# Performance work log

Hardware: AMD Instinct MI355X
Metric: run time of the kernel (lower is better)

Reference implementation:

```python
import jax, jax.numpy as jnp
import numpy as np

ALPHA = 0.1  # leakyRNN default alpha


def setup_inputs() -> dict:
    key = jax.random.key(0)
    k1, k2, k3, k4 = jax.random.split(key, 4)
    B, T, N_in, n, N = 256, 2048, 3, 2, 128
    u = jax.random.normal(k1, (B, T, N_in), dtype=jnp.float32)
    matB = jax.random.uniform(k2, (N, N), dtype=jnp.float32)
    # scaled for recurrence stability over T=2048 steps (spectral radius of 0.9*I + 0.1*W < 1)
    wIn = jax.random.normal(k3, (n, N_in), dtype=jnp.float32) * 0.5
    wRec = jax.random.normal(k4, (n, n), dtype=jnp.float32) * 0.5
    return {"u": u, "matB": matB, "wIn": wIn, "wRec": wRec}


def reference(u, matB, wIn, wRec):
    B, T, _ = u.shape
    n = wRec.shape[0]
    N = matB.shape[0]

    # (bias=False, init_state_train=False -> y0 = 0)
    y0 = jnp.zeros((B, n), dtype=u.dtype)

    def step(y, xt):
        y = (1.0 - ALPHA) * y + ALPHA * (jax.nn.relu(y) @ wRec.T + xt @ wIn.T)
        return y, y

    _, hidden = jax.lax.scan(step, y0, jnp.swapaxes(u, 0, 1))  # [T,B,n]
    hidden = jnp.swapaxes(hidden, 0, 1)  # [B,T,n]

    # ZeroPad1d((0, N-n)) pads the last (feature) dim on the right
    x_padded = jnp.pad(hidden, ((0, 0), (0, 0), (0, N - n)))  # [B,T,N]

    # Orthonormal (Cayley) parametrization: A = B - B^T; Q solves Q @ (I+A) = (I-A)
    A = matB - matB.T
    I = jnp.eye(N, dtype=matB.dtype)
    Q = jnp.linalg.solve((I + A).T, (I - A).T).T  # (I-A) @ inv(I+A)

    # nn.Linear(N, N, bias=False) with weight Q: y = x @ Q^T
    return x_padded @ Q.T
```

## Files before the change

### kernel.cpp

```cpp
#include <hip/hip_runtime.h>

#define TT 2048
#define BATCH 256
#define LDC 132
#define NCOL 130

typedef float vfloat4 __attribute__((ext_vector_type(4)));


__global__ __launch_bounds__(256) void proj_kernel(
    const float* __restrict__ u, const float* __restrict__ wIn, float* __restrict__ ws)
{
    __shared__ float2 tile[64][33];
    const int tid = threadIdx.x;
    const int tb = blockIdx.x & 31;
    const int bb = blockIdx.x >> 5;
    const int t0 = tb * 64;
    const int b0 = bb * 32;

    const float w00 = 0.1f * wIn[0], w01 = 0.1f * wIn[1], w02 = 0.1f * wIn[2];
    const float w10 = 0.1f * wIn[3], w11 = 0.1f * wIn[4], w12 = 0.1f * wIn[5];

    const int tl  = tid & 63;
    const int bl0 = tid >> 6;
#pragma unroll
    for (int s = 0; s < 8; ++s) {
        int bl = bl0 + s * 4;
        const float* p = u + ((size_t)(b0 + bl) * TT + t0 + tl) * 3;
        float x = p[0], y = p[1], z = p[2];
        float2 dv;
        dv.x = fmaf(x, w00, fmaf(y, w01, z * w02));
        dv.y = fmaf(x, w10, fmaf(y, w11, z * w12));
        tile[tl][bl] = dv;
    }
    __syncthreads();

    float* d = ws + 256;
    const int bw  = tid & 31;
    const int tg0 = tid >> 5;
#pragma unroll
    for (int s = 0; s < 2; ++s) {
        int t4l = tg0 + s * 8;
        float2 a0 = tile[t4l * 4 + 0][bw];
        float2 a1 = tile[t4l * 4 + 1][bw];
        float2 a2 = tile[t4l * 4 + 2][bw];
        float2 a3 = tile[t4l * 4 + 3][bw];
        float* p = d + ((size_t)((t0 >> 2) + t4l) * BATCH + (b0 + bw)) * 8;
        vfloat4 w0, w1;
        w0.x = a0.x; w0.y = a0.y; w0.z = a1.x; w0.w = a1.y;
        w1.x = a2.x; w1.y = a2.y; w1.z = a3.x; w1.w = a3.y;
        *(vfloat4*)p       = w0;
        *(vfloat4*)(p + 4) = w1;
    }
}

__global__ __launch_bounds__(256) void ge_rnn_kernel(
    const float* __restrict__ matB, const float* __restrict__ wRec,
    float* __restrict__ ws)
{
    if (blockIdx.x == 0) {
        __shared__ __align__(16) float Mc[NCOL * LDC];
        __shared__ float vb[256];
        const int tid = threadIdx.x;

        for (int e = tid; e < 128 * 128; e += 256) {
            int i = e >> 7, j = e & 127;
            float a = matB[i * 128 + j] - matB[j * 128 + i];
            Mc[j * LDC + i] = a + ((i == j) ? 1.0f : 0.0f);
        }
        for (int i = tid; i < 128; i += 256) {
            Mc[128 * LDC + i] = (i == 0) ? 1.0f : 0.0f;
            Mc[129 * LDC + i] = (i == 1) ? 1.0f : 0.0f;
        }
        __syncthreads();

        for (int k = 0; k < 127; ++k) {
            int j = tid;
            if (j > k && j < NCOL) {
                float scale = Mc[j * LDC + k] / Mc[k * LDC + k];
                int i = k + 1;
                int iv = (i + 3) & ~3;
                if (iv > 128) iv = 128;
                for (; i < iv; ++i)
                    Mc[j * LDC + i] = fmaf(-Mc[k * LDC + i], scale, Mc[j * LDC + i]);
                for (; i < 128; i += 4) {
                    float4 m = *(float4*)&Mc[j * LDC + i];
                    float4 f = *(const float4*)&Mc[k * LDC + i];
                    m.x = fmaf(-f.x, scale, m.x);
                    m.y = fmaf(-f.y, scale, m.y);
                    m.z = fmaf(-f.z, scale, m.z);
                    m.w = fmaf(-f.w, scale, m.w);
                    *(float4*)&Mc[j * LDC + i] = m;
                }
            }
            __syncthreads();
        }

        if (tid < 64) {
            const int l = tid;
            float r0 = Mc[128 * LDC + l],      s0 = Mc[129 * LDC + l];
            float r1 = Mc[128 * LDC + l + 64], s1 = Mc[129 * LDC + l + 64];
            for (int k = 127; k >= 0; --k) {
                float Ukk = Mc[k * LDC + k];
                float c0 = (k >= 64) ? r1 : r0;
                float c1 = (k >= 64) ? s1 : s0;
                float v0 = __shfl(c0, k & 63) / Ukk;
                float v1 = __shfl(c1, k & 63) / Ukk;
                if (l == (k & 63)) { vb[k] = v0; vb[128 + k] = v1; }
                float ul = Mc[k * LDC + l];
                float uh = Mc[k * LDC + l + 64];
                if (l < k)      { r0 = fmaf(-ul, v0, r0); s0 = fmaf(-ul, v1, s0); }
                if (l + 64 < k) { r1 = fmaf(-uh, v0, r1); s1 = fmaf(-uh, v1, s1); }
            }
        }
        __syncthreads();

        if (tid < 128) {
            int i = tid;
            float q0 = vb[i], q1 = vb[128 + i];
            for (int j = 0; j < 128; ++j) {
                float aij = matB[i * 128 + j] - matB[j * 128 + i];
                q0 = fmaf(-aij, vb[j],       q0);
                q1 = fmaf(-aij, vb[128 + j], q1);
            }
            ws[i]       = q0;
            ws[128 + i] = q1;
        }
    } else {
        const int lane = threadIdx.x;
        if (lane >= 64) {
            const int pid = lane - 64;
            const float* dd = ws + 256;
            const size_t boff = (size_t)(blockIdx.x - 1) * 64 * 8;
            float acc = 0.f;
            for (int c = pid; c < 512 * 128; c += 192) {
                int t4 = c >> 7, part = c & 127;
                vfloat4 v = *(const vfloat4*)(dd + (size_t)t4 * (BATCH * 8) + boff + part * 4);
                acc += v.x + v.y + v.z + v.w;
            }
            asm volatile("" :: "v"(acc));
            return;
        }
        const int b = (blockIdx.x - 1) * 64 + lane;
        float* base = ws + 256 + (size_t)b * 8;
        const float a00 = 0.1f * wRec[0], a01 = 0.1f * wRec[1];
        const float a10 = 0.1f * wRec[2], a11 = 0.1f * wRec[3];
        float y0 = 0.f, y1 = 0.f;

        vfloat4 A[16], Bv[16];

#define RNN_STEP(d0, d1) do {                                   \
        float rr0 = fmaxf(y0, 0.f), rr1 = fmaxf(y1, 0.f);       \
        float p0 = fmaf(0.9f, y0, (d0));                        \
        float p1 = fmaf(0.9f, y1, (d1));                        \
        y0 = fmaf(rr1, a01, fmaf(rr0, a00, p0));                \
        y1 = fmaf(rr1, a11, fmaf(rr0, a10, p1));                \
        (d0) = y0; (d1) = y1; } while (0)

        auto LOAD = [&](vfloat4* buf, int g) {
#pragma unroll
            for (int k = 0; k < 8; ++k) {
                const float* p = base + (size_t)(g * 8 + k) * (BATCH * 8);
                buf[2 * k]     = *(const vfloat4*)p;
                buf[2 * k + 1] = *(const vfloat4*)(p + 4);
            }
        };
        auto CSTORE = [&](vfloat4* buf, int g) {
#pragma unroll
            for (int k = 0; k < 8; ++k) {
                vfloat4 v0 = buf[2 * k], v1 = buf[2 * k + 1];
                RNN_STEP(v0.x, v0.y);
                RNN_STEP(v0.z, v0.w);
                RNN_STEP(v1.x, v1.y);
                RNN_STEP(v1.z, v1.w);
                float* p = base + (size_t)(g * 8 + k) * (BATCH * 8);
                *(vfloat4*)p       = v0;
                *(vfloat4*)(p + 4) = v1;
            }
        };

        LOAD(A, 0);
        for (int g = 0; g < 62; g += 2) {
            LOAD(Bv, g + 1);
            CSTORE(A, g);
            LOAD(A, g + 2);
            CSTORE(Bv, g + 1);
        }
        LOAD(Bv, 63);
        CSTORE(A, 62);
        CSTORE(Bv, 63);
#undef RNN_STEP
    }
}

__global__ __launch_bounds__(256) void out_kernel(
    const float* __restrict__ ws, float* __restrict__ out)
{
    const int tid = threadIdx.x;
    const int jg  = tid & 31;
    const int sub = tid >> 5;
    float4 qa = *(const float4*)(ws + jg * 4);
    float4 qb = *(const float4*)(ws + 128 + jg * 4);
    const float* h = ws + 256;
    const int ngroups = BATCH * (TT / 8);
    for (int g = blockIdx.x; g < ngroups; g += gridDim.x) {
        int b = g >> 8;
        int t = (g & 255) * 8 + sub;
        const float* hp = h + ((size_t)(t >> 2) * BATCH + b) * 8 + (t & 3) * 2;
        float2 hv = *(const float2*)hp;
        vfloat4 o;
        o.x = fmaf(hv.x, qa.x, hv.y * qb.x);
        o.y = fmaf(hv.x, qa.y, hv.y * qb.y);
        o.z = fmaf(hv.x, qa.z, hv.y * qb.z);
        o.w = fmaf(hv.x, qa.w, hv.y * qb.w);
        __builtin_nontemporal_store(o, (vfloat4*)(out + ((size_t)b * TT + t) * 128 + jg * 4));
    }
}

extern "C" void kernel_launch(void* const* d_in, const int* in_sizes, int n_in,
                              void* d_out, int out_size, void* d_ws, size_t ws_size,
                              hipStream_t stream) {
    const float* u    = (const float*)d_in[0];
    const float* matB = (const float*)d_in[1];
    const float* wIn  = (const float*)d_in[2];
    const float* wRec = (const float*)d_in[3];
    float* out = (float*)d_out;
    float* ws  = (float*)d_ws;

    hipLaunchKernelGGL(proj_kernel,   dim3(256),  dim3(256), 0, stream, u, wIn, ws);
    hipLaunchKernelGGL(ge_rnn_kernel, dim3(5),    dim3(256), 0, stream, matB, wRec, ws);
    hipLaunchKernelGGL(out_kernel,    dim3(8192), dim3(256), 0, stream, ws, out);
}
```

Before: 542.2 us.

## Swizzle LU shared layout, drop prefetch warps, unroll RNN and output loads

Replaces the padded shared-memory layout of the Gaussian elimination matrix with an XOR-swizzled 128-wide layout to avoid LDS bank conflicts. Removes the helper wavefronts that pre-read the workspace into cache. Replaces the array-based double buffers in the recurrence with named vector registers so nothing spills to scratch. Restructures the output kernel so each block handles 64 timesteps of one batch row, issuing all hidden-state loads before the stores. Dropping the cache-warming wavefronts may expose more memory latency in the serial recurrence.

```diff
diff --git a/kernel.cpp b/kernel.cpp
--- a/kernel.cpp
+++ b/kernel.cpp
@@ -2,11 +2,12 @@
 
 #define TT 2048
 #define BATCH 256
-#define LDC 132
 #define NCOL 130
 
 typedef float vfloat4 __attribute__((ext_vector_type(4)));
 
+
+#define MCI(j, i) ((j) * 128 + (((((i) >> 2) ^ ((j) & 7)) << 2) | ((i) & 3)))
 
 __global__ __launch_bounds__(256) void proj_kernel(
     const float* __restrict__ u, const float* __restrict__ wIn, float* __restrict__ ws)
@@ -54,43 +55,43 @@
     }
 }
 
-__global__ __launch_bounds__(256) void ge_rnn_kernel(
+__global__ __launch_bounds__(256, 1) void ge_rnn_kernel(
     const float* __restrict__ matB, const float* __restrict__ wRec,
     float* __restrict__ ws)
 {
     if (blockIdx.x == 0) {
-        __shared__ __align__(16) float Mc[NCOL * LDC];
+        __shared__ __align__(16) float Mc[NCOL * 128];
         __shared__ float vb[256];
         const int tid = threadIdx.x;
 
         for (int e = tid; e < 128 * 128; e += 256) {
             int i = e >> 7, j = e & 127;
             float a = matB[i * 128 + j] - matB[j * 128 + i];
-            Mc[j * LDC + i] = a + ((i == j) ? 1.0f : 0.0f);
+            Mc[MCI(j, i)] = a + ((i == j) ? 1.0f : 0.0f);
         }
         for (int i = tid; i < 128; i += 256) {
-            Mc[128 * LDC + i] = (i == 0) ? 1.0f : 0.0f;
-            Mc[129 * LDC + i] = (i == 1) ? 1.0f : 0.0f;
+            Mc[MCI(128, i)] = (i == 0) ? 1.0f : 0.0f;
+            Mc[MCI(129, i)] = (i == 1) ? 1.0f : 0.0f;
         }
         __syncthreads();
 
         for (int k = 0; k < 127; ++k) {
             int j = tid;
             if (j > k && j < NCOL) {
-                float scale = Mc[j * LDC + k] / Mc[k * LDC + k];
+                float scale = Mc[MCI(j, k)] / Mc[MCI(k, k)];
                 int i = k + 1;
                 int iv = (i + 3) & ~3;
                 if (iv > 128) iv = 128;
                 for (; i < iv; ++i)
-                    Mc[j * LDC + i] = fmaf(-Mc[k * LDC + i], scale, Mc[j * LDC + i]);
+                    Mc[MCI(j, i)] = fmaf(-Mc[MCI(k, i)], scale, Mc[MCI(j, i)]);
                 for (; i < 128; i += 4) {
-                    float4 m = *(float4*)&Mc[j * LDC + i];
-                    float4 f = *(const float4*)&Mc[k * LDC + i];
+                    float4 m = *(float4*)&Mc[MCI(j, i)];
+                    float4 f = *(const float4*)&Mc[MCI(k, i)];
                     m.x = fmaf(-f.x, scale, m.x);
                     m.y = fmaf(-f.y, scale, m.y);
                     m.z = fmaf(-f.z, scale, m.z);
                     m.w = fmaf(-f.w, scale, m.w);
-                    *(float4*)&Mc[j * LDC + i] = m;
+                    *(float4*)&Mc[MCI(j, i)] = m;
                 }
             }
             __syncthreads();
@@ -98,17 +99,17 @@
 
         if (tid < 64) {
             const int l = tid;
-            float r0 = Mc[128 * LDC + l],      s0 = Mc[129 * LDC + l];
-            float r1 = Mc[128 * LDC + l + 64], s1 = Mc[129 * LDC + l + 64];
+            float r0 = Mc[MCI(128, l)],      s0 = Mc[MCI(129, l)];
+            float r1 = Mc[MCI(128, l + 64)], s1 = Mc[MCI(129, l + 64)];
             for (int k = 127; k >= 0; --k) {
-                float Ukk = Mc[k * LDC + k];
+                float Ukk = Mc[MCI(k, k)];
                 float c0 = (k >= 64) ? r1 : r0;
                 float c1 = (k >= 64) ? s1 : s0;
                 float v0 = __shfl(c0, k & 63) / Ukk;
                 float v1 = __shfl(c1, k & 63) / Ukk;
                 if (l == (k & 63)) { vb[k] = v0; vb[128 + k] = v1; }
-                float ul = Mc[k * LDC + l];
-                float uh = Mc[k * LDC + l + 64];
+                float ul = Mc[MCI(k, l)];
+                float uh = Mc[MCI(k, l + 64)];
                 if (l < k)      { r0 = fmaf(-ul, v0, r0); s0 = fmaf(-ul, v1, s0); }
                 if (l + 64 < k) { r1 = fmaf(-uh, v0, r1); s1 = fmaf(-uh, v1, s1); }
             }
@@ -128,26 +129,15 @@
         }
     } else {
         const int lane = threadIdx.x;
-        if (lane >= 64) {
-            const int pid = lane - 64;
-            const float* dd = ws + 256;
-            const size_t boff = (size_t)(blockIdx.x - 1) * 64 * 8;
-            float acc = 0.f;
-            for (int c = pid; c < 512 * 128; c += 192) {
-                int t4 = c >> 7, part = c & 127;
-                vfloat4 v = *(const vfloat4*)(dd + (size_t)t4 * (BATCH * 8) + boff + part * 4);
-                acc += v.x + v.y + v.z + v.w;
-            }
-            asm volatile("" :: "v"(acc));
-            return;
-        }
+        if (lane >= 64) return;
         const int b = (blockIdx.x - 1) * 64 + lane;
         float* base = ws + 256 + (size_t)b * 8;
         const float a00 = 0.1f * wRec[0], a01 = 0.1f * wRec[1];
         const float a10 = 0.1f * wRec[2], a11 = 0.1f * wRec[3];
         float y0 = 0.f, y1 = 0.f;
 
-        vfloat4 A[16], Bv[16];
+        vfloat4 A0, A1, A2, A3, A4, A5, A6, A7, A8, A9, A10, A11, A12, A13, A14, A15;
+        vfloat4 B0, B1, B2, B3, B4, B5, B6, B7, B8, B9, B10, B11, B12, B13, B14, B15;
 
 #define RNN_STEP(d0, d1) do {                                   \
         float rr0 = fmaxf(y0, 0.f), rr1 = fmaxf(y1, 0.f);       \
@@ -157,39 +147,50 @@
         y1 = fmaf(rr1, a11, fmaf(rr0, a10, p1));                \
         (d0) = y0; (d1) = y1; } while (0)
 
-        auto LOAD = [&](vfloat4* buf, int g) {
-#pragma unroll
-            for (int k = 0; k < 8; ++k) {
-                const float* p = base + (size_t)(g * 8 + k) * (BATCH * 8);
-                buf[2 * k]     = *(const vfloat4*)p;
-                buf[2 * k + 1] = *(const vfloat4*)(p + 4);
-            }
-        };
-        auto CSTORE = [&](vfloat4* buf, int g) {
-#pragma unroll
-            for (int k = 0; k < 8; ++k) {
-                vfloat4 v0 = buf[2 * k], v1 = buf[2 * k + 1];
-                RNN_STEP(v0.x, v0.y);
-                RNN_STEP(v0.z, v0.w);
-                RNN_STEP(v1.x, v1.y);
-                RNN_STEP(v1.z, v1.w);
-                float* p = base + (size_t)(g * 8 + k) * (BATCH * 8);
-                *(vfloat4*)p       = v0;
-                *(vfloat4*)(p + 4) = v1;
-            }
-        };
-
-        LOAD(A, 0);
-        for (int g = 0; g < 62; g += 2) {
-            LOAD(Bv, g + 1);
-            CSTORE(A, g);
-            LOAD(A, g + 2);
-            CSTORE(Bv, g + 1);
-        }
-        LOAD(Bv, 63);
-        CSTORE(A, 62);
-        CSTORE(Bv, 63);
+#define LOAD16(V, g) do { \
+        const float* _p = base + (size_t)(g) * (8 * BATCH * 8); \
+        V##0  = *(const vfloat4*)(_p + 0 * 2048); V##1  = *(const vfloat4*)(_p + 0 * 2048 + 4); \
+        V##2  = *(const vfloat4*)(_p + 1 * 2048); V##3  = *(const vfloat4*)(_p + 1 * 2048 + 4); \
+        V##4  = *(const vfloat4*)(_p + 2 * 2048); V##5  = *(const vfloat4*)(_p + 2 * 2048 + 4); \
+        V##6  = *(const vfloat4*)(_p + 3 * 2048); V##7  = *(const vfloat4*)(_p + 3 * 2048 + 4); \
+        V##8  = *(const vfloat4*)(_p + 4 * 2048); V##9  = *(const vfloat4*)(_p + 4 * 2048 + 4); \
+        V##10 = *(const vfloat4*)(_p + 5 * 2048); V##11 = *(const vfloat4*)(_p + 5 * 2048 + 4); \
+        V##12 = *(const vfloat4*)(_p + 6 * 2048); V##13 = *(const vfloat4*)(_p + 6 * 2048 + 4); \
+        V##14 = *(const vfloat4*)(_p + 7 * 2048); V##15 = *(const vfloat4*)(_p + 7 * 2048 + 4); \
+    } while (0)
+
+#define PAIR(Va, Vb, q, off) do { \
+        RNN_STEP(Va.x, Va.y); RNN_STEP(Va.z, Va.w); \
+        RNN_STEP(Vb.x, Vb.y); RNN_STEP(Vb.z, Vb.w); \
+        *(vfloat4*)((q) + (off)) = Va; *(vfloat4*)((q) + (off) + 4) = Vb; \
+    } while (0)
+
+#define CSTORE16(V, g) do { \
+        float* _q = base + (size_t)(g) * (8 * BATCH * 8); \
+        PAIR(V##0,  V##1,  _q, 0 * 2048); \
+        PAIR(V##2,  V##3,  _q, 1 * 2048); \
+        PAIR(V##4,  V##5,  _q, 2 * 2048); \
+        PAIR(V##6,  V##7,  _q, 3 * 2048); \
+        PAIR(V##8,  V##9,  _q, 4 * 2048); \
+        PAIR(V##10, V##11, _q, 5 * 2048); \
+        PAIR(V##12, V##13, _q, 6 * 2048); \
+        PAIR(V##14, V##15, _q, 7 * 2048); \
+    } while (0)
+
+        LOAD16(A, 0);
+        for (int g = 0; g <= 60; g += 2) {
+            LOAD16(B, g + 1);
+            CSTORE16(A, g);
+            LOAD16(A, g + 2);
+            CSTORE16(B, g + 1);
+        }
+        LOAD16(B, 63);
+        CSTORE16(A, 62);
+        CSTORE16(B, 63);
 #undef RNN_STEP
+#undef LOAD16
+#undef PAIR
+#undef CSTORE16
     }
 }
 
@@ -202,19 +203,27 @@
     float4 qa = *(const float4*)(ws + jg * 4);
     float4 qb = *(const float4*)(ws + 128 + jg * 4);
     const float* h = ws + 256;
-    const int ngroups = BATCH * (TT / 8);
-    for (int g = blockIdx.x; g < ngroups; g += gridDim.x) {
-        int b = g >> 8;
-        int t = (g & 255) * 8 + sub;
-        const float* hp = h + ((size_t)(t >> 2) * BATCH + b) * 8 + (t & 3) * 2;
-        float2 hv = *(const float2*)hp;
-        vfloat4 o;
-        o.x = fmaf(hv.x, qa.x, hv.y * qb.x);
-        o.y = fmaf(hv.x, qa.y, hv.y * qb.y);
-        o.z = fmaf(hv.x, qa.z, hv.y * qb.z);
-        o.w = fmaf(hv.x, qa.w, hv.y * qb.w);
-        __builtin_nontemporal_store(o, (vfloat4*)(out + ((size_t)b * TT + t) * 128 + jg * 4));
-    }
+
+    const int b  = blockIdx.x >> 5;
+    const int t0 = (blockIdx.x & 31) * 64;
+
+    float2 hv0, hv1, hv2, hv3, hv4, hv5, hv6, hv7;
+#define HLOAD(R, i) do { int t = t0 + (i) * 8 + sub; \
+        R = *(const float2*)(h + ((size_t)(t >> 2) * BATCH + b) * 8 + (t & 3) * 2); } while (0)
+    HLOAD(hv0, 0); HLOAD(hv1, 1); HLOAD(hv2, 2); HLOAD(hv3, 3);
+    HLOAD(hv4, 4); HLOAD(hv5, 5); HLOAD(hv6, 6); HLOAD(hv7, 7);
+#undef HLOAD
+
+#define OSTORE(R, i) do { int t = t0 + (i) * 8 + sub; \
+        vfloat4 o; \
+        o.x = fmaf(R.x, qa.x, R.y * qb.x); \
+        o.y = fmaf(R.x, qa.y, R.y * qb.y); \
+        o.z = fmaf(R.x, qa.z, R.y * qb.z); \
+        o.w = fmaf(R.x, qa.w, R.y * qb.w); \
+        __builtin_nontemporal_store(o, (vfloat4*)(out + ((size_t)b * TT + t) * 128 + jg * 4)); } while (0)
+    OSTORE(hv0, 0); OSTORE(hv1, 1); OSTORE(hv2, 2); OSTORE(hv3, 3);
+    OSTORE(hv4, 4); OSTORE(hv5, 5); OSTORE(hv6, 6); OSTORE(hv7, 7);
+#undef OSTORE
 }
 
 extern "C" void kernel_launch(void* const* d_in, const int* in_sizes, int n_in,
```

Measured after the change: 518.5 us. -4.4%, faster.
